# Performance work log

Measured on AMD Instinct MI355X. Metric: run time of the kernel, lower is better.

The kernel has to match this reference:

```python
import jax, jax.numpy as jnp
import numpy as np

OUT_FEATURES = 4096
IN_FEATURES = 4096
R = 16
DIST = 4
N_FREQ = 10000
SCALING = 150.0


def setup_inputs() -> dict:
    key = jax.random.key(0)
    k_x, k_w, k_b, k_s, k_a, k_i = jax.random.split(key, 6)
    x = jax.random.normal(k_x, (4, 2048, IN_FEATURES), dtype=jnp.float32)
    base_w = jax.random.normal(k_w, (OUT_FEATURES, IN_FEATURES), dtype=jnp.float32) * 0.02
    base_b = jax.random.normal(k_b, (OUT_FEATURES,), dtype=jnp.float32) * 0.02
    spectrum = jax.random.normal(k_s, (N_FREQ,), dtype=jnp.float32)
    hora_A = jax.random.normal(k_a, (R, IN_FEATURES), dtype=jnp.float32)
    # torch uses randperm(r*out_features)[:n_frequency] -> unique flat indices
    idx = jax.random.permutation(k_i, R * OUT_FEATURES)[:N_FREQ].astype(jnp.int32)
    return {"x": x, "base_w": base_w, "base_b": base_b,
            "spectrum": spectrum, "hora_A": hora_A, "idx": idx}


def reference(x, base_w, base_b, spectrum, hora_A, idx):
    # --- get_delta_weight ---
    rows = idx // R            # index into out_features
    cols = idx % R             # index into r
    dense_spectrum = jnp.zeros((OUT_FEATURES, R), dtype=spectrum.dtype)
    dense_spectrum = dense_spectrum.at[rows, cols].set(spectrum)
    # chunk_size = ceil(out/dist) = 1024; out divisible by dist -> pure reshape
    chunks = dense_spectrum.reshape(DIST, OUT_FEATURES // DIST, R)
    B = jnp.fft.ifft2(chunks, axes=(-2, -1)).real.astype(spectrum.dtype)
    B = B.reshape(OUT_FEATURES, R)
    delta_w = (B * SCALING) @ hora_A          # [out_features, in_features]
    # --- forward: base linear + adapter linear ---
    base_out = jnp.einsum('bsi,oi->bso', x, base_w) + base_b
    result = base_out + jnp.einsum('bsi,oi->bso', x, delta_w)
    return result
```

## Files before the change

### kernel.cpp

```cpp
#include <hip/hip_runtime.h>
#include <hip/hip_bf16.h>


#define OUTF 4096
#define INF  4096
#define NFREQ 10000
#define MDIM 8192
#define KT   (INF / 64)
#define NX4  ((MDIM * INF) / 4)

typedef __attribute__((ext_vector_type(8))) short bf16x8;
typedef __attribute__((ext_vector_type(4))) float f32x4;

__device__ __forceinline__ unsigned int bf16pack2(float a, float b) {
    unsigned int ua = __builtin_bit_cast(unsigned int, a);
    unsigned int ub = __builtin_bit_cast(unsigned int, b);
    ua = (ua + 0x7fffu + ((ua >> 16) & 1u)) >> 16;
    ub = (ub + 0x7fffu + ((ub >> 16) & 1u)) & 0xffff0000u;
    return ua | ub;
}

__device__ __forceinline__ void async_copy16(const void* g, void* l) {
    __builtin_amdgcn_global_load_lds(
        (__attribute__((address_space(1))) void*)(g),
        (__attribute__((address_space(3))) void*)(l),
        16, 0, 0);
}

__global__ __launch_bounds__(256) void k1_compact_cvt_kernel(
        const float* __restrict__ spectrum, const int* __restrict__ idx,
        int2* __restrict__ cjk2, int* __restrict__ boff,
        const float4* __restrict__ x4, uint2* __restrict__ xb) {
    __shared__ int2 s_list[4096];
    __shared__ int  wcnt[4];
    __shared__ int  s_cnt;
    __shared__ int  kcnt[16];
    __shared__ int  kbase[17];
    const int tid = threadIdx.x;
    if (blockIdx.x >= 4) {
        for (int i = (blockIdx.x - 4) * 256 + tid; i < NX4; i += 2044 * 256) {
            float4 v = x4[i];
            xb[i] = make_uint2(bf16pack2(v.x, v.y), bf16pack2(v.z, v.w));
        }
        return;
    }
    const int p  = blockIdx.x;
    const int wv = tid >> 6, ln = tid & 63;
    int cnt = 0;
    for (int i0 = wv * 64; i0 < NFREQ; i0 += 256) {
        const int i = i0 + ln;
        bool m = (i < NFREQ) && ((idx[i] >> 14) == p);
        cnt += __popcll(__ballot(m));
    }
    if (ln == 0) wcnt[wv] = cnt;
    __syncthreads();
    int base = 0;
    for (int w = 0; w < wv; ++w) base += wcnt[w];
    for (int i0 = wv * 64; i0 < NFREQ; i0 += 256) {
        const int i = i0 + ln;
        bool m = false; int id = 0;
        if (i < NFREQ) { id = idx[i]; m = ((id >> 14) == p); }
        unsigned long long bal = __ballot(m);
        if (m) {
            int pos = base + __popcll(bal & ((1ull << ln) - 1ull));
            if (pos < 4096)
                s_list[pos] = make_int2(id & 16383,
                                        __builtin_bit_cast(int, spectrum[i]));
        }
        base += __popcll(bal);
    }
    if (tid == 0) {
        int t = wcnt[0] + wcnt[1] + wcnt[2] + wcnt[3];
        s_cnt = (t < 4096) ? t : 4096;
    }
    __syncthreads();
    const int n = s_cnt;
    for (int q = 0; q < 4; ++q) {
        const int k = wv * 4 + q;
        int c = 0;
        for (int t0 = 0; t0 < n; t0 += 64) {
            const int t = t0 + ln;
            bool m = (t < n) && ((s_list[t].x & 15) == k);
            c += __popcll(__ballot(m));
        }
        if (ln == 0) kcnt[k] = c;
    }
    __syncthreads();
    if (tid == 0) {
        int a = 0;
        for (int k = 0; k < 16; ++k) { kbase[k] = a; a += kcnt[k]; }
        kbase[16] = a;
    }
    __syncthreads();
    for (int q = 0; q < 4; ++q) {
        const int k = wv * 4 + q;
        int b2 = kbase[k];
        for (int t0 = 0; t0 < n; t0 += 64) {
            const int t = t0 + ln;
            bool m = (t < n) && ((s_list[t].x & 15) == k);
            unsigned long long bal = __ballot(m);
            if (m) {
                int pos = b2 + __popcll(bal & ((1ull << ln) - 1ull));
                cjk2[p * 4096 + pos] = make_int2(s_list[t].x >> 4, s_list[t].y);
            }
            b2 += __popcll(bal);
        }
    }
    if (tid < 17) boff[p * 17 + tid] = kbase[tid];
}

__global__ __launch_bounds__(256) void k2_w_kernel(
        const int2* __restrict__ cjk2, const int* __restrict__ boff,
        const float* __restrict__ bw, const float* __restrict__ A,
        unsigned short* __restrict__ W) {
    __shared__ int2  s_jv[4096];
    __shared__ float s1re[8][16];
    __shared__ float s1im[8][17];
    __shared__ float sB[8][17];
    const int tid = threadIdx.x;
    const int n0  = blockIdx.x * 8;
    const int p   = n0 >> 10;
    const int cnt = boff[p * 17 + 16];
    for (int t = tid; t < cnt; t += 256) s_jv[t] = cjk2[p * 4096 + t];
    __syncthreads();
    if (tid < 128) {
        const int m_loc = tid >> 4;
        const int k     = tid & 15;
        const int m     = (n0 & 1023) + m_loc;
        const int kb0   = boff[p * 17 + k];
        const int kb1   = boff[p * 17 + k + 1];
        const float c1  = 6.283185307179586f / 1024.f;
        float re = 0.f, im = 0.f;
        for (int t = kb0; t < kb1; ++t) {
            const int2 jv = s_jv[t];
            const float v = __builtin_bit_cast(float, jv.y);
            const float ang = (float)((jv.x * m) & 1023) * c1;
            re += v * __cosf(ang);
            im += v * __sinf(ang);
        }
        s1re[m_loc][k] = re;
        s1im[m_loc][k] = im;
    }
    __syncthreads();
    if (tid < 128) {
        const int m_loc = tid >> 4;
        const int r     = tid & 15;
        const float c2  = 6.283185307179586f / 16.f;
        float b = 0.f;
#pragma unroll
        for (int k2 = 0; k2 < 16; ++k2) {
            const float ang = (float)((k2 * r) & 15) * c2;
            b += s1re[m_loc][k2] * __cosf(ang) - s1im[m_loc][k2] * __sinf(ang);
        }
        sB[m_loc][r] = b * (150.f / 16384.f);
    }
    __syncthreads();
    const float4* A4  = (const float4*)A;
    const float4* bw4 = (const float4*)bw;
    uint2* W2 = (uint2*)W;
#pragma unroll 1
    for (int q = 0; q < 4; ++q) {
        const int c4 = tid + q * 256;
        float4 a[16];
#pragma unroll
        for (int r = 0; r < 16; ++r) a[r] = A4[r * 1024 + c4];
#pragma unroll 1
        for (int nn = 0; nn < 8; ++nn) {
            const int n = n0 + nn;
            float4 wv = bw4[n * 1024 + c4];
#pragma unroll
            for (int r = 0; r < 16; ++r) {
                float s = sB[nn][r];
                wv.x += s * a[r].x; wv.y += s * a[r].y;
                wv.z += s * a[r].z; wv.w += s * a[r].w;
            }
            W2[n * 1024 + c4] = make_uint2(bf16pack2(wv.x, wv.y),
                                           bf16pack2(wv.z, wv.w));
        }
    }
}

__global__ __launch_bounds__(512, 2) void gemm256_kernel(
        const unsigned short* __restrict__ Xb,
        const unsigned short* __restrict__ Wb,
        const float* __restrict__ bias, float* __restrict__ C) {
    __shared__ __align__(1024) char lds[131072];

    const int tid  = threadIdx.x;
    const int lane = tid & 63;
    const int wid  = tid >> 6;
    const int wm   = wid >> 2;
    const int wn   = wid & 3;

    int bid = blockIdx.x;
    bid = (bid & 7) * 64 + (bid >> 3);
    const int tm = bid >> 4;
    const int tn = bid & 15;
    const int arow0 = tm * 256;
    const int brow0 = tn * 256;

    const int srow  = tid >> 3;
    const int scole = (((tid & 7) * 16) ^ ((srow & 7) << 4)) >> 1;
    const int sldsb = tid * 16;

    const int l15 = lane & 15;
    const int kx0 = ((lane >> 4) * 16) ^ ((lane & 7) << 4);
    const int kx1 = kx0 ^ 64;
    const int abase0 = (wm * 128 + l15) * 128;
    const int bbase0 = 32768 + (wn * 64 + l15) * 128;

    f32x4 acc[8][4] = {};
    bf16x8 af[4][2], bfa[2][2], bfb[2][2];

#define STAGE_HALF(mat, grow0, t, ldsbase) do {                               \
        const unsigned short* _s =                                            \
            (mat) + ((grow0) + srow) * INF + (t) * 64 + scole;                \
        async_copy16(_s, lds + (ldsbase) + sldsb);                            \
        async_copy16(_s + 64 * INF, lds + (ldsbase) + 8192 + sldsb);          \
    } while (0)

#define LDA(DB, m, kh) (*(const bf16x8*)(lds + (DB) + abase0 + (m) * 2048 + ((kh) ? kx1 : kx0)))
#define LDB(DB, n, kh) (*(const bf16x8*)(lds + (DB) + bbase0 + (n) * 2048 + ((kh) ? kx1 : kx0)))
#define MFMA(a, b, c) __builtin_amdgcn_mfma_f32_16x16x32_bf16((a), (b), (c), 0, 0, 0)
#define BARRIER() do { asm volatile("" ::: "memory");                         \
                       __builtin_amdgcn_s_barrier();                          \
                       asm volatile("" ::: "memory"); } while (0)

#define QMFMA(mh, BF)                                                         \
    __builtin_amdgcn_s_setprio(1);                                            \
    _Pragma("unroll") for (int ks = 0; ks < 2; ++ks)                          \
        _Pragma("unroll") for (int m = 0; m < 4; ++m)                         \
            _Pragma("unroll") for (int n = 0; n < 2; ++n)                     \
                acc[(mh) * 4 + m][(BF) * 2 + n] =                             \
                    MFMA(af[m][ks], ((BF) ? bfb : bfa)[n][ks],                \
                         acc[(mh) * 4 + m][(BF) * 2 + n]);                    \
    __builtin_amdgcn_s_setprio(0)

#define RD_AF(DB, mh)                                                         \
    _Pragma("unroll") for (int m = 0; m < 4; ++m) {                           \
        af[m][0] = LDA(DB, (mh) * 4 + m, 0);                                  \
        af[m][1] = LDA(DB, (mh) * 4 + m, 1); }
#define RD_BFA(DB)                                                            \
    _Pragma("unroll") for (int n = 0; n < 2; ++n) {                           \
        bfa[n][0] = LDB(DB, n, 0); bfa[n][1] = LDB(DB, n, 1); }
#define RD_BFB(DB)                                                            \
    _Pragma("unroll") for (int n = 0; n < 2; ++n) {                           \
        bfb[n][0] = LDB(DB, n + 2, 0); bfb[n][1] = LDB(DB, n + 2, 1); }

#define PAIR(CUR, OTH, s) do {                                                \
                              \
    RD_BFA(CUR); RD_AF(CUR, 0);                                               \
    STAGE_HALF(Xb, arow0 + 128, (s) + 1, (OTH) + 16384);                      \
    QMFMA(0, 0); BARRIER();                                                   \
                                   \
    RD_BFB(CUR);                                                              \
    STAGE_HALF(Wb, brow0 + 128, (s) + 1, (OTH) + 49152);                      \
    QMFMA(0, 1); BARRIER();                                                   \
                             \
    RD_AF(CUR, 1);                                                            \
    if ((s) + 2 < KT) STAGE_HALF(Wb, brow0, (s) + 2, (CUR) + 32768);          \
    QMFMA(1, 0); BARRIER();                                                   \
             \
    if ((s) + 2 < KT) STAGE_HALF(Xb, arow0, (s) + 2, (CUR) + 0);              \
    QMFMA(1, 1);                                                              \
    if ((s) + 2 < KT) { asm volatile("s_waitcnt vmcnt(4)" ::: "memory"); }    \
    else              { asm volatile("s_waitcnt vmcnt(0)" ::: "memory"); }    \
    BARRIER();                                                                \
                         \
    RD_BFA(OTH); RD_AF(OTH, 0);                                               \
    if ((s) + 2 < KT) STAGE_HALF(Xb, arow0 + 128, (s) + 2, (CUR) + 16384);    \
    QMFMA(0, 0); BARRIER();                                                   \
                              \
    RD_BFB(OTH);                                                              \
    if ((s) + 2 < KT) STAGE_HALF(Wb, brow0 + 128, (s) + 2, (CUR) + 49152);    \
    QMFMA(0, 1); BARRIER();                                                   \
                             \
    RD_AF(OTH, 1);                                                            \
    if ((s) + 3 < KT) STAGE_HALF(Wb, brow0, (s) + 3, (OTH) + 32768);          \
    QMFMA(1, 0); BARRIER();                                                   \
           \
    if ((s) + 3 < KT) STAGE_HALF(Xb, arow0, (s) + 3, (OTH) + 0);              \
    QMFMA(1, 1);                                                              \
    if ((s) + 3 < KT) { asm volatile("s_waitcnt vmcnt(4)" ::: "memory"); }    \
    else              { asm volatile("s_waitcnt vmcnt(0)" ::: "memory"); }    \
    BARRIER();                                                                \
} while (0)

    STAGE_HALF(Wb, brow0,       0, 32768);
    STAGE_HALF(Xb, arow0,       0, 0);
    STAGE_HALF(Xb, arow0 + 128, 0, 16384);
    STAGE_HALF(Wb, brow0 + 128, 0, 49152);
    STAGE_HALF(Wb, brow0,       1, 65536 + 32768);
    STAGE_HALF(Xb, arow0,       1, 65536 + 0);
    asm volatile("s_waitcnt vmcnt(4)" ::: "memory");
    BARRIER();

    for (int s = 0; s < KT; s += 2)
        PAIR(0, 65536, s);

#pragma unroll
    for (int n = 0; n < 4; ++n) {
        const int gcol = brow0 + wn * 64 + n * 16 + l15;
        const float bv = bias[gcol];
#pragma unroll
        for (int m = 0; m < 8; ++m) {
            const int grow = arow0 + wm * 128 + m * 16 + (lane >> 4) * 4;
#pragma unroll
            for (int rg = 0; rg < 4; ++rg)
                C[(grow + rg) * OUTF + gcol] = acc[m][n][rg] + bv;
        }
    }
#undef STAGE_HALF
#undef LDA
#undef LDB
#undef MFMA
#undef BARRIER
#undef QMFMA
#undef RD_AF
#undef RD_BFA
#undef RD_BFB
#undef PAIR
}

extern "C" void kernel_launch(void* const* d_in, const int* in_sizes, int n_in,
                              void* d_out, int out_size, void* d_ws, size_t ws_size,
                              hipStream_t stream) {
    const float* x    = (const float*)d_in[0];
    const float* bw   = (const float*)d_in[1];
    const float* bb   = (const float*)d_in[2];
    const float* spec = (const float*)d_in[3];
    const float* ha   = (const float*)d_in[4];
    const int*   idx  = (const int*)d_in[5];
    float* out = (float*)d_out;

    char* ws = (char*)d_ws;
    unsigned short* Wb   = (unsigned short*)ws;
    unsigned short* Xb   = (unsigned short*)(ws + 33554432);
    int2*           cjk2 = (int2*)(ws + 100663296);
    int*            boff = (int*)(ws + 100794368);

    k1_compact_cvt_kernel<<<2048, 256, 0, stream>>>(
        spec, idx, cjk2, boff, (const float4*)x, (uint2*)Xb);
    k2_w_kernel<<<512, 256, 0, stream>>>(cjk2, boff, bw, ha, Wb);
    gemm256_kernel<<<512, 512, 0, stream>>>(Xb, Wb, bb, out);
}
```

Measured before the change: 375.2 us.

## Fuse spectrum compaction, x conversion and weight build into one cooperative kernel

Merges the compaction/x-conversion kernel and the delta-weight kernel into a single cooperative-launch kernel of 1024 blocks separated by a grid-wide sync. Three quarters of the x-to-bf16 conversion runs before the sync and the remainder runs on the idle blocks afterwards, so it overlaps with the weight construction. The weight build also loads hora_A in two halves of 8 rows to cut register pressure, allowing 4 blocks per CU. This removes one kernel launch boundary, but adds the cost of a grid sync and relies on all 1024 blocks being co-resident.

```diff
diff --git a/kernel.cpp b/kernel.cpp
--- a/kernel.cpp
+++ b/kernel.cpp
@@ -1,5 +1,6 @@
 #include <hip/hip_runtime.h>
 #include <hip/hip_bf16.h>
+#include <hip/hip_cooperative_groups.h>
 
 
 #define OUTF 4096
@@ -8,6 +9,7 @@
 #define MDIM 8192
 #define KT   (INF / 64)
 #define NX4  ((MDIM * INF) / 4)
+#define SPLIT ((NX4 / 4) * 3)
 
 typedef __attribute__((ext_vector_type(8))) short bf16x8;
 typedef __attribute__((ext_vector_type(4))) float f32x4;
@@ -27,101 +29,108 @@
         16, 0, 0);
 }
 
-__global__ __launch_bounds__(256) void k1_compact_cvt_kernel(
+__global__ __launch_bounds__(256, 4) void prep_coop_kernel(
         const float* __restrict__ spectrum, const int* __restrict__ idx,
         int2* __restrict__ cjk2, int* __restrict__ boff,
+        const float* __restrict__ bw, const float* __restrict__ A,
+        unsigned short* __restrict__ W,
         const float4* __restrict__ x4, uint2* __restrict__ xb) {
-    __shared__ int2 s_list[4096];
-    __shared__ int  wcnt[4];
-    __shared__ int  s_cnt;
-    __shared__ int  kcnt[16];
-    __shared__ int  kbase[17];
-    const int tid = threadIdx.x;
-    if (blockIdx.x >= 4) {
-        for (int i = (blockIdx.x - 4) * 256 + tid; i < NX4; i += 2044 * 256) {
-            float4 v = x4[i];
-            xb[i] = make_uint2(bf16pack2(v.x, v.y), bf16pack2(v.z, v.w));
-        }
-        return;
-    }
-    const int p  = blockIdx.x;
-    const int wv = tid >> 6, ln = tid & 63;
-    int cnt = 0;
-    for (int i0 = wv * 64; i0 < NFREQ; i0 += 256) {
-        const int i = i0 + ln;
-        bool m = (i < NFREQ) && ((idx[i] >> 14) == p);
-        cnt += __popcll(__ballot(m));
-    }
-    if (ln == 0) wcnt[wv] = cnt;
-    __syncthreads();
-    int base = 0;
-    for (int w = 0; w < wv; ++w) base += wcnt[w];
-    for (int i0 = wv * 64; i0 < NFREQ; i0 += 256) {
-        const int i = i0 + ln;
-        bool m = false; int id = 0;
-        if (i < NFREQ) { id = idx[i]; m = ((id >> 14) == p); }
-        unsigned long long bal = __ballot(m);
-        if (m) {
-            int pos = base + __popcll(bal & ((1ull << ln) - 1ull));
-            if (pos < 4096)
-                s_list[pos] = make_int2(id & 16383,
-                                        __builtin_bit_cast(int, spectrum[i]));
-        }
-        base += __popcll(bal);
-    }
-    if (tid == 0) {
-        int t = wcnt[0] + wcnt[1] + wcnt[2] + wcnt[3];
-        s_cnt = (t < 4096) ? t : 4096;
-    }
-    __syncthreads();
-    const int n = s_cnt;
-    for (int q = 0; q < 4; ++q) {
-        const int k = wv * 4 + q;
-        int c = 0;
-        for (int t0 = 0; t0 < n; t0 += 64) {
-            const int t = t0 + ln;
-            bool m = (t < n) && ((s_list[t].x & 15) == k);
-            c += __popcll(__ballot(m));
-        }
-        if (ln == 0) kcnt[k] = c;
-    }
-    __syncthreads();
-    if (tid == 0) {
-        int a = 0;
-        for (int k = 0; k < 16; ++k) { kbase[k] = a; a += kcnt[k]; }
-        kbase[16] = a;
-    }
-    __syncthreads();
-    for (int q = 0; q < 4; ++q) {
-        const int k = wv * 4 + q;
-        int b2 = kbase[k];
-        for (int t0 = 0; t0 < n; t0 += 64) {
-            const int t = t0 + ln;
-            bool m = (t < n) && ((s_list[t].x & 15) == k);
-            unsigned long long bal = __ballot(m);
-            if (m) {
-                int pos = b2 + __popcll(bal & ((1ull << ln) - 1ull));
-                cjk2[p * 4096 + pos] = make_int2(s_list[t].x >> 4, s_list[t].y);
-            }
-            b2 += __popcll(bal);
-        }
-    }
-    if (tid < 17) boff[p * 17 + tid] = kbase[tid];
-}
-
-__global__ __launch_bounds__(256) void k2_w_kernel(
-        const int2* __restrict__ cjk2, const int* __restrict__ boff,
-        const float* __restrict__ bw, const float* __restrict__ A,
-        unsigned short* __restrict__ W) {
-    __shared__ int2  s_jv[4096];
+    __shared__ int2  s_list[4096];
+    __shared__ int   wcnt[4];
+    __shared__ int   s_cnt;
+    __shared__ int   kcnt[16];
+    __shared__ int   kbase[17];
     __shared__ float s1re[8][16];
     __shared__ float s1im[8][17];
     __shared__ float sB[8][17];
     const int tid = threadIdx.x;
-    const int n0  = blockIdx.x * 8;
+    const int bid = blockIdx.x;
+
+    if (bid >= 4) {
+        for (int i = (bid - 4) * 256 + tid; i < SPLIT; i += 1020 * 256) {
+            float4 v = x4[i];
+            xb[i] = make_uint2(bf16pack2(v.x, v.y), bf16pack2(v.z, v.w));
+        }
+    } else {
+        const int p  = bid;
+        const int wv = tid >> 6, ln = tid & 63;
+        int cnt = 0;
+        for (int i0 = wv * 64; i0 < NFREQ; i0 += 256) {
+            const int i = i0 + ln;
+            bool m = (i < NFREQ) && ((idx[i] >> 14) == p);
+            cnt += __popcll(__ballot(m));
+        }
+        if (ln == 0) wcnt[wv] = cnt;
+        __syncthreads();
+        int base = 0;
+        for (int w = 0; w < wv; ++w) base += wcnt[w];
+        for (int i0 = wv * 64; i0 < NFREQ; i0 += 256) {
+            const int i = i0 + ln;
+            bool m = false; int id = 0;
+            if (i < NFREQ) { id = idx[i]; m = ((id >> 14) == p); }
+            unsigned long long bal = __ballot(m);
+            if (m) {
+                int pos = base + __popcll(bal & ((1ull << ln) - 1ull));
+                if (pos < 4096)
+                    s_list[pos] = make_int2(id & 16383,
+                                            __builtin_bit_cast(int, spectrum[i]));
+            }
+            base += __popcll(bal);
+        }
+        if (tid == 0) {
+            int t = wcnt[0] + wcnt[1] + wcnt[2] + wcnt[3];
+            s_cnt = (t < 4096) ? t : 4096;
+        }
+        __syncthreads();
+        const int n = s_cnt;
+        for (int q = 0; q < 4; ++q) {
+            const int k = wv * 4 + q;
+            int c = 0;
+            for (int t0 = 0; t0 < n; t0 += 64) {
+                const int t = t0 + ln;
+                bool m = (t < n) && ((s_list[t].x & 15) == k);
+                c += __popcll(__ballot(m));
+            }
+            if (ln == 0) kcnt[k] = c;
+        }
+        __syncthreads();
+        if (tid == 0) {
+            int a = 0;
+            for (int k = 0; k < 16; ++k) { kbase[k] = a; a += kcnt[k]; }
+            kbase[16] = a;
+        }
+        __syncthreads();
+        for (int q = 0; q < 4; ++q) {
+            const int k = wv * 4 + q;
+            int b2 = kbase[k];
+            for (int t0 = 0; t0 < n; t0 += 64) {
+                const int t = t0 + ln;
+                bool m = (t < n) && ((s_list[t].x & 15) == k);
+                unsigned long long bal = __ballot(m);
+                if (m) {
+                    int pos = b2 + __popcll(bal & ((1ull << ln) - 1ull));
+                    cjk2[p * 4096 + pos] =
+                        make_int2(s_list[t].x >> 4, s_list[t].y);
+                }
+                b2 += __popcll(bal);
+            }
+        }
+        if (tid < 17) boff[p * 17 + tid] = kbase[tid];
+    }
+
+    cooperative_groups::this_grid().sync();
+
+    if (bid >= 512) {
+        for (int i = (bid - 512) * 256 + tid + SPLIT; i < NX4; i += 512 * 256) {
+            float4 v = x4[i];
+            xb[i] = make_uint2(bf16pack2(v.x, v.y), bf16pack2(v.z, v.w));
+        }
+        return;
+    }
+    const int n0  = bid * 8;
     const int p   = n0 >> 10;
     const int cnt = boff[p * 17 + 16];
-    for (int t = tid; t < cnt; t += 256) s_jv[t] = cjk2[p * 4096 + t];
+    for (int t = tid; t < cnt; t += 256) s_list[t] = cjk2[p * 4096 + t];
     __syncthreads();
     if (tid < 128) {
         const int m_loc = tid >> 4;
@@ -132,7 +141,7 @@
         const float c1  = 6.283185307179586f / 1024.f;
         float re = 0.f, im = 0.f;
         for (int t = kb0; t < kb1; ++t) {
-            const int2 jv = s_jv[t];
+            const int2 jv = s_list[t];
             const float v = __builtin_bit_cast(float, jv.y);
             const float ang = (float)((jv.x * m) & 1023) * c1;
             re += v * __cosf(ang);
@@ -161,18 +170,21 @@
 #pragma unroll 1
     for (int q = 0; q < 4; ++q) {
         const int c4 = tid + q * 256;
-        float4 a[16];
-#pragma unroll
-        for (int r = 0; r < 16; ++r) a[r] = A4[r * 1024 + c4];
 #pragma unroll 1
         for (int nn = 0; nn < 8; ++nn) {
             const int n = n0 + nn;
             float4 wv = bw4[n * 1024 + c4];
-#pragma unroll
-            for (int r = 0; r < 16; ++r) {
-                float s = sB[nn][r];
-                wv.x += s * a[r].x; wv.y += s * a[r].y;
-                wv.z += s * a[r].z; wv.w += s * a[r].w;
+#pragma unroll 1
+            for (int rh = 0; rh < 2; ++rh) {
+                float4 a[8];
+#pragma unroll
+                for (int r = 0; r < 8; ++r) a[r] = A4[(rh * 8 + r) * 1024 + c4];
+#pragma unroll
+                for (int r = 0; r < 8; ++r) {
+                    float s = sB[nn][rh * 8 + r];
+                    wv.x += s * a[r].x; wv.y += s * a[r].y;
+                    wv.z += s * a[r].z; wv.w += s * a[r].w;
+                }
             }
             W2[n * 1024 + c4] = make_uint2(bf16pack2(wv.x, wv.y),
                                            bf16pack2(wv.z, wv.w));
@@ -248,37 +260,29 @@
         bfb[n][0] = LDB(DB, n + 2, 0); bfb[n][1] = LDB(DB, n + 2, 1); }
 
 #define PAIR(CUR, OTH, s) do {                                                \
-                              \
     RD_BFA(CUR); RD_AF(CUR, 0);                                               \
     STAGE_HALF(Xb, arow0 + 128, (s) + 1, (OTH) + 16384);                      \
     QMFMA(0, 0); BARRIER();                                                   \
-                                   \
     RD_BFB(CUR);                                                              \
     STAGE_HALF(Wb, brow0 + 128, (s) + 1, (OTH) + 49152);                      \
     QMFMA(0, 1); BARRIER();                                                   \
-                             \
     RD_AF(CUR, 1);                                                            \
     if ((s) + 2 < KT) STAGE_HALF(Wb, brow0, (s) + 2, (CUR) + 32768);          \
     QMFMA(1, 0); BARRIER();                                                   \
-             \
     if ((s) + 2 < KT) STAGE_HALF(Xb, arow0, (s) + 2, (CUR) + 0);              \
     QMFMA(1, 1);                                                              \
     if ((s) + 2 < KT) { asm volatile("s_waitcnt vmcnt(4)" ::: "memory"); }    \
     else              { asm volatile("s_waitcnt vmcnt(0)" ::: "memory"); }    \
     BARRIER();                                                                \
-                         \
     RD_BFA(OTH); RD_AF(OTH, 0);                                               \
     if ((s) + 2 < KT) STAGE_HALF(Xb, arow0 + 128, (s) + 2, (CUR) + 16384);    \
     QMFMA(0, 0); BARRIER();                                                   \
-                              \
     RD_BFB(OTH);                                                              \
     if ((s) + 2 < KT) STAGE_HALF(Wb, brow0 + 128, (s) + 2, (CUR) + 49152);    \
     QMFMA(0, 1); BARRIER();                                                   \
-                             \
     RD_AF(OTH, 1);                                                            \
     if ((s) + 3 < KT) STAGE_HALF(Wb, brow0, (s) + 3, (OTH) + 32768);          \
     QMFMA(1, 0); BARRIER();                                                   \
-           \
     if ((s) + 3 < KT) STAGE_HALF(Xb, arow0, (s) + 3, (OTH) + 0);              \
     QMFMA(1, 1);                                                              \
     if ((s) + 3 < KT) { asm volatile("s_waitcnt vmcnt(4)" ::: "memory"); }    \
@@ -339,8 +343,13 @@
     int2*           cjk2 = (int2*)(ws + 100663296);
     int*            boff = (int*)(ws + 100794368);
 
-    k1_compact_cvt_kernel<<<2048, 256, 0, stream>>>(
-        spec, idx, cjk2, boff, (const float4*)x, (uint2*)Xb);
-    k2_w_kernel<<<512, 256, 0, stream>>>(cjk2, boff, bw, ha, Wb);
+    const float4* x4p = (const float4*)x;
+    uint2*        xbp = (uint2*)Xb;
+    void* args[] = {
+        (void*)&spec, (void*)&idx, (void*)&cjk2, (void*)&boff,
+        (void*)&bw, (void*)&ha, (void*)&Wb, (void*)&x4p, (void*)&xbp
+    };
+    hipLaunchCooperativeKernel((const void*)prep_coop_kernel,
+                               dim3(1024), dim3(256), args, 0, stream);
     gemm256_kernel<<<512, 512, 0, stream>>>(Xb, Wb, bb, out);
 }
```

Result: slower. 530.5 us (+41.4%).
